# Optimization experiments

Measured on AMD Instinct MI355X. Metric: run time of the kernel, lower is better.

The kernel has to match this reference:

```python
import jax, jax.numpy as jnp
import numpy as np

B, S, I, H, N_ODE = 256, 64, 256, 1024, 4


def setup_inputs() -> dict:
    key = jax.random.key(0)
    ks = jax.random.split(key, 6)
    x = jax.random.normal(ks[0], (B, S, I), dtype=jnp.float32)
    t = jnp.arange(S, dtype=jnp.float32) * 0.1  # increasing observation times
    W_in = jax.random.normal(ks[1], (H, I), dtype=jnp.float32) / np.float32(np.sqrt(I))
    b_in = jnp.zeros((H,), dtype=jnp.float32)
    W_h = jax.random.normal(ks[2], (H, H), dtype=jnp.float32) / np.float32(np.sqrt(H))
    b_h = jnp.zeros((H,), dtype=jnp.float32)
    W_ode = jax.random.normal(ks[3], (H, H), dtype=jnp.float32) / np.float32(np.sqrt(H))
    b_ode = jnp.zeros((H,), dtype=jnp.float32)
    return {"x": x, "t": t, "W_in": W_in, "b_in": b_in, "W_h": W_h,
            "b_h": b_h, "W_ode": W_ode, "b_ode": b_ode}


def reference(x, t, W_in, b_in, W_h, b_h, W_ode, b_ode):
    # x: [B, S, I], t: [S]. ODE-RNN: per timestep, evolve h by N_ODE Euler
    # steps of dh/dt = tanh(W_ode h + b_ode) over [t_{i-1}, t_i], then
    # h = tanh(W_in x_i + b_in + W_h h + b_h). First step has dt = 0
    # (original uses t[i] for both endpoints when i == 0).
    t_prev = jnp.concatenate([t[:1], t[:-1]])
    dts = t - t_prev  # [S]

    def step(h, inp):
        x_i, dt = inp  # x_i: [B, I], dt: scalar
        dth = dt / N_ODE
        def euler(hc, _):
            return hc + dth * jnp.tanh(hc @ W_ode.T + b_ode), None
        h, _ = jax.lax.scan(euler, h, None, length=N_ODE)
        h = jnp.tanh(x_i @ W_in.T + b_in + h @ W_h.T + b_h)
        return h, None

    h0 = jnp.zeros((x.shape[0], W_h.shape[0]), dtype=x.dtype)
    xs = jnp.swapaxes(x, 0, 1)  # [S, B, I]
    h_final, _ = jax.lax.scan(step, h0, (xs, dts))
    return h_final  # [B, H]
```

## Files before the change

kernel.cpp:

```cpp
#include <hip/hip_runtime.h>

#define B_ 256
#define S_ 64
#define I_ 256
#define H_ 1024
#define NODE_ 4
#define NB 256
#define NG 16
#define GSZ 16

typedef __attribute__((ext_vector_type(8))) short short8;
typedef __attribute__((ext_vector_type(4))) float f32x4;

__device__ __forceinline__ short f2bf(float f) {
    unsigned u = __float_as_uint(f);
    u += 0x7fffu + ((u >> 16) & 1u);
    return (short)(u >> 16);
}
__device__ __forceinline__ unsigned pack2(float a, float b) {
    return (unsigned)(unsigned short)f2bf(a) | ((unsigned)(unsigned short)f2bf(b) << 16);
}

__device__ __forceinline__ float ftanh(float x) {
    float e = __expf(2.0f * fabsf(x));
    float r = __builtin_fmaf(-2.0f, __builtin_amdgcn_rcpf(e + 1.0f), 1.0f);
    return copysignf(r, x);
}

__device__ __forceinline__ void gbar_slow(unsigned* cnt, unsigned target) {
    __syncthreads();
    if (threadIdx.x == 0) {
        __hip_atomic_fetch_add(cnt, 1u, __ATOMIC_RELAXED, __HIP_MEMORY_SCOPE_AGENT);
        while (__hip_atomic_load(cnt, __ATOMIC_RELAXED, __HIP_MEMORY_SCOPE_AGENT) < target)
            __builtin_amdgcn_s_sleep(1);
    }
    __syncthreads();
}

__global__ __launch_bounds__(256, 1)
void odernn_persist(const float* __restrict__ x, const float* __restrict__ t,
                    const float* __restrict__ W_in, const float* __restrict__ b_in,
                    const float* __restrict__ W_h, const float* __restrict__ b_h,
                    const float* __restrict__ W_ode, const float* __restrict__ b_ode,
                    float* __restrict__ out,
                    unsigned short* __restrict__ h0buf, unsigned short* __restrict__ h1buf,
                    unsigned short* __restrict__ Whbf, unsigned short* __restrict__ Winbf,
                    unsigned* __restrict__ cnts)
{
    __shared__ short Wlds[64 * 1024];
    __shared__ short Hlds[16 * 1024];

    const int tid = threadIdx.x;
    const int blk = blockIdx.x;
    const int bi = blk & 15;
    const int bj = blk >> 4;
    const int lane = tid & 63;
    const int wv = tid >> 6;
    const int r16 = lane & 15, kg = lane >> 4;

    {
        const int g = blk * 256 + tid;
        const float* src = W_h + (size_t)g * 16;
        unsigned* dst = (unsigned*)Whbf + (size_t)g * 8;
#pragma unroll
        for (int i = 0; i < 4; ++i) {
            float4 v = *(const float4*)(src + i * 4);
            __hip_atomic_store(dst + i * 2,     pack2(v.x, v.y), __ATOMIC_RELAXED, __HIP_MEMORY_SCOPE_AGENT);
            __hip_atomic_store(dst + i * 2 + 1, pack2(v.z, v.w), __ATOMIC_RELAXED, __HIP_MEMORY_SCOPE_AGENT);
        }
        float4 v = *(const float4*)(W_in + (size_t)g * 4);
        unsigned* d2 = (unsigned*)Winbf + (size_t)g * 2;
        __hip_atomic_store(d2,     pack2(v.x, v.y), __ATOMIC_RELAXED, __HIP_MEMORY_SCOPE_AGENT);
        __hip_atomic_store(d2 + 1, pack2(v.z, v.w), __ATOMIC_RELAXED, __HIP_MEMORY_SCOPE_AGENT);
    }

    {
        const int c = tid >> 2;
        const int ks = (tid & 3) * 256;
        const float* wsrc = W_ode + (size_t)(bj * 64 + c) * H_ + ks;
        for (int i = 0; i < 32; ++i) {
            float4 v0 = *(const float4*)(wsrc + i * 8);
            float4 v1 = *(const float4*)(wsrc + i * 8 + 4);
            short8 sv = { f2bf(v0.x), f2bf(v0.y), f2bf(v0.z), f2bf(v0.w),
                          f2bf(v1.x), f2bf(v1.y), f2bf(v1.z), f2bf(v1.w) };
            int idx = c * 1024 + ks + i * 8;
            *(short8*)&Wlds[idx ^ ((c & 7) << 3)] = sv;
        }
    }

    const int row0  = bi * 16 + kg * 4;
    const int arowg = bi * 16 + r16;
    const int col   = bj * 64 + wv * 16 + r16;
    const int wbrow = wv * 16 + r16;

    const char* aBase = (const char*)Hlds + r16 * 2048;
    const int hswz = (r16 & 7) << 4;

    const float bodec = b_ode[col];
    const float binc  = b_in[col] + b_h[col];

    f32x4 hreg = {0.f, 0.f, 0.f, 0.f};
#pragma unroll
    for (int r = 0; r < 4; ++r)
        __hip_atomic_store(&h0buf[(size_t)(row0 + r) * H_ + col], (unsigned short)0,
                           __ATOMIC_RELAXED, __HIP_MEMORY_SCOPE_AGENT);

    gbar_slow(&cnts[512], NB);

    unsigned* flags = cnts + 1024 + bi * 32;
    unsigned ep = 1;

    const int srow = tid >> 4, scl = tid & 15;
    const int swz_w = (srow & 7) << 4;
    auto stage = [&](const unsigned short* hsrc) {
        const unsigned long long* src =
            (const unsigned long long*)(hsrc + (size_t)bi * 16 * H_) + srow * 256 + scl;
        unsigned long long v[16];
#pragma unroll
        for (int j = 0; j < 16; ++j)
            v[j] = __hip_atomic_load(src + j * 16, __ATOMIC_RELAXED, __HIP_MEMORY_SCOPE_AGENT);
#pragma unroll
        for (int j = 0; j < 16; ++j) {
            int byte = (scl * 8 + j * 128) ^ swz_w;
            *(unsigned long long*)((char*)Hlds + srow * 2048 + byte) = v[j];
        }
        __syncthreads();
    };

    auto publish_barrier = [&](unsigned short* dst, f32x4 pv, unsigned epoch) {
#pragma unroll
        for (int r = 0; r < 4; ++r)
            __hip_atomic_store(&dst[(size_t)(row0 + r) * H_ + col],
                               (unsigned short)f2bf(pv[r]),
                               __ATOMIC_RELAXED, __HIP_MEMORY_SCOPE_AGENT);
        __syncthreads();
        if (tid == 0)
            __hip_atomic_store(&flags[bj], epoch, __ATOMIC_RELAXED, __HIP_MEMORY_SCOPE_AGENT);
        if (wv == 0) {
            const unsigned* fp = flags + (lane & 15);
            for (;;) {
                unsigned v = __hip_atomic_load(fp, __ATOMIC_RELAXED, __HIP_MEMORY_SCOPE_AGENT);
                if (__all((int)(v >= epoch))) break;
                __builtin_amdgcn_s_sleep(1);
            }
        }
        __syncthreads();
    };

    const unsigned short* hin = h0buf;
    unsigned short* hout = h1buf;

    for (int s = 0; s < S_; ++s) {
        if (s > 0) {
            const float dth = (t[s] - t[s - 1]) * 0.25f;
            for (int e = 0; e < NODE_; ++e) {
                stage(hin);
                f32x4 acc0 = {0.f, 0.f, 0.f, 0.f}, acc1 = {0.f, 0.f, 0.f, 0.f};
#pragma unroll
                for (int k0 = 0; k0 < H_; k0 += 64) {
                    short8 a0 = *(const short8*)(aBase + (((k0 + kg * 8) * 2) ^ hswz));
                    short8 b0 = *(const short8*)&Wlds[(wbrow * 1024 + k0 + kg * 8) ^ ((wbrow & 7) << 3)];
                    acc0 = __builtin_amdgcn_mfma_f32_16x16x32_bf16(a0, b0, acc0, 0, 0, 0);
                    short8 a1 = *(const short8*)(aBase + (((k0 + 32 + kg * 8) * 2) ^ hswz));
                    short8 b1 = *(const short8*)&Wlds[(wbrow * 1024 + k0 + 32 + kg * 8) ^ ((wbrow & 7) << 3)];
                    acc1 = __builtin_amdgcn_mfma_f32_16x16x32_bf16(a1, b1, acc1, 0, 0, 0);
                }
                f32x4 acc = acc0 + acc1;
#pragma unroll
                for (int r = 0; r < 4; ++r)
                    hreg[r] += dth * ftanh(acc[r] + bodec);
                publish_barrier(hout, hreg, ep); ++ep;
                const unsigned short* tmp = hin; hin = hout; hout = (unsigned short*)tmp;
            }
        }
        {
            stage(hin);
            const unsigned short* whB = Whbf + (size_t)col * H_ + kg * 8;
            f32x4 acc0 = {0.f, 0.f, 0.f, 0.f}, acc1 = {0.f, 0.f, 0.f, 0.f};
#pragma unroll
            for (int k0 = 0; k0 < H_; k0 += 64) {
                short8 a0 = *(const short8*)(aBase + (((k0 + kg * 8) * 2) ^ hswz));
                short8 b0 = *(const short8*)(whB + k0);
                acc0 = __builtin_amdgcn_mfma_f32_16x16x32_bf16(a0, b0, acc0, 0, 0, 0);
                short8 a1 = *(const short8*)(aBase + (((k0 + 32 + kg * 8) * 2) ^ hswz));
                short8 b1 = *(const short8*)(whB + k0 + 32);
                acc1 = __builtin_amdgcn_mfma_f32_16x16x32_bf16(a1, b1, acc1, 0, 0, 0);
            }
            const float* xB = x + ((size_t)arowg * S_ + s) * I_ + kg * 8;
            const unsigned short* wiB = Winbf + (size_t)col * I_ + kg * 8;
#pragma unroll
            for (int k2 = 0; k2 < I_; k2 += 64) {
                float4 a0f = *(const float4*)(xB + k2);
                float4 a1f = *(const float4*)(xB + k2 + 4);
                short8 a = { f2bf(a0f.x), f2bf(a0f.y), f2bf(a0f.z), f2bf(a0f.w),
                             f2bf(a1f.x), f2bf(a1f.y), f2bf(a1f.z), f2bf(a1f.w) };
                short8 b = *(const short8*)(wiB + k2);
                acc0 = __builtin_amdgcn_mfma_f32_16x16x32_bf16(a, b, acc0, 0, 0, 0);
                float4 a2f = *(const float4*)(xB + k2 + 32);
                float4 a3f = *(const float4*)(xB + k2 + 36);
                short8 a2 = { f2bf(a2f.x), f2bf(a2f.y), f2bf(a2f.z), f2bf(a2f.w),
                              f2bf(a3f.x), f2bf(a3f.y), f2bf(a3f.z), f2bf(a3f.w) };
                short8 b2 = *(const short8*)(wiB + k2 + 32);
                acc1 = __builtin_amdgcn_mfma_f32_16x16x32_bf16(a2, b2, acc1, 0, 0, 0);
            }
            f32x4 acc = acc0 + acc1;
            const bool last = (s == S_ - 1);
            f32x4 hv;
#pragma unroll
            for (int r = 0; r < 4; ++r) {
                hv[r] = ftanh(acc[r] + binc);
                hreg[r] = hv[r];
            }
            if (last) {
#pragma unroll
                for (int r = 0; r < 4; ++r)
                    out[(size_t)(row0 + r) * H_ + col] = hv[r];
            } else {
                publish_barrier(hout, hv, ep); ++ep;
                const unsigned short* tmp = hin; hin = hout; hout = (unsigned short*)tmp;
            }
        }
    }
}

extern "C" void kernel_launch(void* const* d_in, const int* in_sizes, int n_in,
                              void* d_out, int out_size, void* d_ws, size_t ws_size,
                              hipStream_t stream) {
    const float* x     = (const float*)d_in[0];
    const float* t     = (const float*)d_in[1];
    const float* W_in  = (const float*)d_in[2];
    const float* b_in  = (const float*)d_in[3];
    const float* W_h   = (const float*)d_in[4];
    const float* b_h   = (const float*)d_in[5];
    const float* W_ode = (const float*)d_in[6];
    const float* b_ode = (const float*)d_in[7];

    unsigned short* h0    = (unsigned short*)d_ws;
    unsigned short* h1    = h0 + (size_t)B_ * H_;
    unsigned short* Whbf  = h1 + (size_t)B_ * H_;
    unsigned short* Winbf = Whbf + (size_t)H_ * H_;
    unsigned* cnts = (unsigned*)(Winbf + (size_t)H_ * I_);

    (void)hipMemsetAsync(cnts, 0, (1024 + NG * 32) * sizeof(unsigned), stream);

    odernn_persist<<<dim3(NB), dim3(256), 0, stream>>>(
        x, t, W_in, b_in, W_h, b_h, W_ode, b_ode,
        (float*)d_out, h0, h1, Whbf, Winbf, cnts);
}
```

Baseline: 1.283 ms.

## Replace post-publish barrier with per-chunk flag-gated staging of hidden state

Publishing no longer waits for all 16 producer blocks in the row group, and the trailing __syncthreads is dropped. Instead, the staging step polls the producer flags and loads each 64-column chunk of h as soon as the block that owns it has published the current epoch. This overlaps loading the chunks that are ready with waiting on slower producers, and takes the full group barrier off the critical path. The double-buffer reuse still looks safe, because a block only overwrites a buffer after every producer has signalled that it finished the step that read it. In exchange there is more flag polling inside the staging loop, and the ordering relies on relaxed atomics.

New measurement: 1.265 ms. No clear change (-1.4%).

```diff
diff --git a/kernel.cpp b/kernel.cpp
--- a/kernel.cpp
+++ b/kernel.cpp
@@ -108,26 +108,37 @@
     gbar_slow(&cnts[512], NB);
 
     unsigned* flags = cnts + 1024 + bi * 32;
-    unsigned ep = 1;
+    unsigned ep = 0;
 
     const int srow = tid >> 4, scl = tid & 15;
     const int swz_w = (srow & 7) << 4;
-    auto stage = [&](const unsigned short* hsrc) {
-        const unsigned long long* src =
+
+    auto stage_gated = [&](const unsigned short* hsrc, unsigned epoch) {
+        const unsigned long long* base =
             (const unsigned long long*)(hsrc + (size_t)bi * 16 * H_) + srow * 256 + scl;
         unsigned long long v[16];
-#pragma unroll
-        for (int j = 0; j < 16; ++j)
-            v[j] = __hip_atomic_load(src + j * 16, __ATOMIC_RELAXED, __HIP_MEMORY_SCOPE_AGENT);
-#pragma unroll
-        for (int j = 0; j < 16; ++j) {
-            int byte = (scl * 8 + j * 128) ^ swz_w;
-            *(unsigned long long*)((char*)Hlds + srow * 2048 + byte) = v[j];
+        unsigned ready = 0;
+#pragma unroll
+        for (int p = 0; p < 16; ++p) {
+            while (!(ready & (1u << p))) {
+                unsigned fv = __hip_atomic_load(&flags[lane & 15],
+                                                __ATOMIC_RELAXED, __HIP_MEMORY_SCOPE_AGENT);
+                unsigned long long b = __ballot((int)(fv >= epoch));
+                ready = (unsigned)(b & 0xFFFFu);
+                if (!(ready & (1u << p))) __builtin_amdgcn_s_sleep(1);
+            }
+            asm volatile("" ::: "memory");
+            v[p] = __hip_atomic_load(base + p * 16, __ATOMIC_RELAXED, __HIP_MEMORY_SCOPE_AGENT);
+        }
+#pragma unroll
+        for (int p = 0; p < 16; ++p) {
+            int byte = ((p * 16 + scl) * 8) ^ swz_w;
+            *(unsigned long long*)((char*)Hlds + srow * 2048 + byte) = v[p];
         }
         __syncthreads();
     };
 
-    auto publish_barrier = [&](unsigned short* dst, f32x4 pv, unsigned epoch) {
+    auto publish = [&](unsigned short* dst, f32x4 pv, unsigned newep) {
 #pragma unroll
         for (int r = 0; r < 4; ++r)
             __hip_atomic_store(&dst[(size_t)(row0 + r) * H_ + col],
@@ -135,16 +146,7 @@
                                __ATOMIC_RELAXED, __HIP_MEMORY_SCOPE_AGENT);
         __syncthreads();
         if (tid == 0)
-            __hip_atomic_store(&flags[bj], epoch, __ATOMIC_RELAXED, __HIP_MEMORY_SCOPE_AGENT);
-        if (wv == 0) {
-            const unsigned* fp = flags + (lane & 15);
-            for (;;) {
-                unsigned v = __hip_atomic_load(fp, __ATOMIC_RELAXED, __HIP_MEMORY_SCOPE_AGENT);
-                if (__all((int)(v >= epoch))) break;
-                __builtin_amdgcn_s_sleep(1);
-            }
-        }
-        __syncthreads();
+            __hip_atomic_store(&flags[bj], newep, __ATOMIC_RELAXED, __HIP_MEMORY_SCOPE_AGENT);
     };
 
     const unsigned short* hin = h0buf;
@@ -154,7 +156,7 @@
         if (s > 0) {
             const float dth = (t[s] - t[s - 1]) * 0.25f;
             for (int e = 0; e < NODE_; ++e) {
-                stage(hin);
+                stage_gated(hin, ep);
                 f32x4 acc0 = {0.f, 0.f, 0.f, 0.f}, acc1 = {0.f, 0.f, 0.f, 0.f};
 #pragma unroll
                 for (int k0 = 0; k0 < H_; k0 += 64) {
@@ -169,12 +171,12 @@
 #pragma unroll
                 for (int r = 0; r < 4; ++r)
                     hreg[r] += dth * ftanh(acc[r] + bodec);
-                publish_barrier(hout, hreg, ep); ++ep;
+                publish(hout, hreg, ep + 1); ++ep;
                 const unsigned short* tmp = hin; hin = hout; hout = (unsigned short*)tmp;
             }
         }
         {
-            stage(hin);
+            stage_gated(hin, ep);
             const unsigned short* whB = Whbf + (size_t)col * H_ + kg * 8;
             f32x4 acc0 = {0.f, 0.f, 0.f, 0.f}, acc1 = {0.f, 0.f, 0.f, 0.f};
 #pragma unroll
@@ -216,7 +218,7 @@
                 for (int r = 0; r < 4; ++r)
                     out[(size_t)(row0 + r) * H_ + col] = hv[r];
             } else {
-                publish_barrier(hout, hv, ep); ++ep;
+                publish(hout, hv, ep + 1); ++ep;
                 const unsigned short* tmp = hin; hin = hout; hout = (unsigned short*)tmp;
             }
         }
```
